# Optimization experiments

Measured on AMD Instinct MI355X. Metric: run time of the kernel, lower is better.

## Reference

```python
import jax, jax.numpy as jnp
import numpy as np

N = 100000      # nodes
E = 1600000     # edges (avg degree 16)
F_N, F_E, H = 5, 3, 64
L = 3           # num GCN layers


def setup_inputs() -> dict:
    key = jax.random.key(0)
    ks = jax.random.split(key, 20)
    s = 0.05
    p = lambda k, shape: jax.random.normal(k, shape, jnp.float32) * s
    return {
        "x": jax.random.normal(ks[0], (N, F_N), jnp.float32),
        "edge_index": jax.random.randint(ks[1], (2, E), 0, N, dtype=jnp.int32),
        "edge_attr": jax.random.normal(ks[2], (E, F_E), jnp.float32),
        # node / edge encoders
        "Wn": p(ks[3], (F_N, H)), "bn": jnp.zeros((H,), jnp.float32),
        "We": p(ks[4], (F_E, H)), "be": jnp.zeros((H,), jnp.float32),
        # stacked GCNConv weights [L, H, H] and biases [L, H]
        "Wc": p(ks[5], (L, H, H)), "bc": jnp.zeros((L, H), jnp.float32),
        # demand forecast head
        "Wd1": p(ks[6], (H, H // 2)), "bd1": jnp.zeros((H // 2,), jnp.float32),
        "Wd2": p(ks[7], (H // 2, 1)), "bd2": jnp.zeros((1,), jnp.float32),
        # inventory optimizer head
        "Wi1": p(ks[8], (H, H // 2)), "bi1": jnp.zeros((H // 2,), jnp.float32),
        "Wi2": p(ks[9], (H // 2, 1)), "bi2": jnp.zeros((1,), jnp.float32),
    }


def reference(x, edge_index, edge_attr, Wn, bn, We, be, Wc, bc,
              Wd1, bd1, Wd2, bd2, Wi1, bi1, Wi2, bi2):
    src, dst = edge_index[0], edge_index[1]
    n = x.shape[0]

    h = jax.nn.relu(x @ Wn + bn)                      # [N, H]
    _ea = jax.nn.relu(edge_attr @ We + be)            # encoded edge feats (GCNConv ignores them)

    # GCN symmetric normalization with self-loops: deg[i] = in_degree(i) + 1
    ones_e = jnp.ones(src.shape[0], h.dtype)
    deg = jax.ops.segment_sum(ones_e, dst, num_segments=n) + 1.0
    dinv = jax.lax.rsqrt(deg)                         # [N]
    norm_e = dinv[src] * dinv[dst]                    # [E]
    norm_self = (dinv * dinv)[:, None]                # [N, 1]

    for l in range(Wc.shape[0]):
        hw = h @ Wc[l]                                # [N, H]
        msgs = norm_e[:, None] * hw[src]              # gather + scale, [E, H]
        agg = jax.ops.segment_sum(msgs, dst, num_segments=n) + norm_self * hw
        h = jax.nn.relu(agg + bc[l])

    demand = jax.nn.relu(h @ Wd1 + bd1) @ Wd2 + bd2   # [N, 1]
    inventory = jax.nn.relu(h @ Wi1 + bi1) @ Wi2 + bi2
    return demand, inventory
```

## Files before the change

### kernel.cpp

```cpp
#include <hip/hip_runtime.h>

#define H 64
#define FN 5
#define EPB 4096
#define BSHIFT 8
#define CAP2 4864

typedef _Float16 half4 __attribute__((ext_vector_type(4)));
typedef _Float16 half8 __attribute__((ext_vector_type(8)));
typedef float    float8v __attribute__((ext_vector_type(8)));

__global__ void k_bscatter2(const int* __restrict__ src, const int* __restrict__ dst,
                            int* __restrict__ lofs_g, int* __restrict__ bcounts,
                            int* __restrict__ binned, int nE, int nbB) {
    __shared__ int lh[512], lpos[512], lcur[512], tmp[256];
    __shared__ int stage[EPB];
    int t = threadIdx.x;
    int e0 = blockIdx.x * EPB;
    int es[16], ed[16];
    lh[t] = 0; lh[t + 256] = 0;
    __syncthreads();
#pragma unroll
    for (int i = 0; i < 16; ++i) {
        int e = e0 + i * 256 + t;
        bool v = e < nE;
        es[i] = v ? src[e] : 0;
        ed[i] = v ? dst[e] : -1;
        if (v) atomicAdd(&lh[ed[i] >> BSHIFT], 1);
    }
    __syncthreads();
    int a0 = lh[2 * t], a1 = lh[2 * t + 1];
    tmp[t] = a0 + a1;
    __syncthreads();
    for (int s = 1; s < 256; s <<= 1) {
        int a = (t >= s) ? tmp[t - s] : 0;
        __syncthreads();
        tmp[t] += a;
        __syncthreads();
    }
    int ex = tmp[t] - (a0 + a1);
    lpos[2 * t] = ex;
    lpos[2 * t + 1] = ex + a0;
    __syncthreads();
    lcur[t] = lpos[t]; lcur[t + 256] = lpos[t + 256];
    size_t row = (size_t)blockIdx.x * (nbB + 1);
    for (int b = t; b <= nbB; b += 256) lofs_g[row + b] = lpos[b];
    for (int b = t; b < nbB; b += 256) if (lh[b]) atomicAdd(&bcounts[b], lh[b]);
    __syncthreads();
#pragma unroll
    for (int i = 0; i < 16; ++i) {
        if (ed[i] >= 0) {
            int b = ed[i] >> BSHIFT;
            int p = atomicAdd(&lcur[b], 1);
            stage[p] = es[i] | ((ed[i] & 255) << 17);
        }
    }
    __syncthreads();
    int total = lpos[nbB];
    for (int j = t; j < total; j += 256) binned[e0 + j] = stage[j];
}

__global__ void k_bscan2(const int* __restrict__ bcounts, int* __restrict__ bbase, int nbB) {
    __shared__ int tmp[512];
    int t = threadIdx.x;
    int v = (t < nbB) ? bcounts[t] : 0;
    tmp[t] = v;
    __syncthreads();
    for (int s = 1; s < 512; s <<= 1) {
        int a = (t >= s) ? tmp[t - s] : 0;
        __syncthreads();
        tmp[t] += a;
        __syncthreads();
    }
    if (t < nbB) bbase[t + 1] = tmp[t];
    if (t == 0) bbase[0] = 0;
}

__global__ void k_bcsr2(const int* __restrict__ binned, const int* __restrict__ lofs_g,
                        const int* __restrict__ bbase, int* __restrict__ row_ptr,
                        int* __restrict__ csr_src, float* __restrict__ dinv,
                        int n, int nE, int nbE, int nbB) {
    __shared__ int len_s[512], start_s[512], roff[512], tmp[256];
    __shared__ int deg[256], st[256], cur[256];
    __shared__ int lbuf[CAP2];
    __shared__ int stage2[CAP2];
    int t = threadIdx.x;
    int B = blockIdx.x;
    int node0 = B << BSHIFT;
    int nn = min(256, n - node0);
    len_s[t] = 0; len_s[t + 256] = 0;
    __syncthreads();
    for (int sb = t; sb < nbE; sb += 256) {
        size_t row = (size_t)sb * (nbB + 1);
        int o0 = lofs_g[row + B], o1 = lofs_g[row + B + 1];
        len_s[sb] = o1 - o0;
        start_s[sb] = sb * EPB + o0;
    }
    __syncthreads();
    int a0 = len_s[2 * t], a1 = len_s[2 * t + 1];
    tmp[t] = a0 + a1;
    __syncthreads();
    for (int s = 1; s < 256; s <<= 1) {
        int a = (t >= s) ? tmp[t - s] : 0;
        __syncthreads();
        tmp[t] += a;
        __syncthreads();
    }
    int ex = tmp[t] - (a0 + a1);
    roff[2 * t] = ex;
    roff[2 * t + 1] = ex + a0;
    __syncthreads();
    int total = min(roff[511] + len_s[511], CAP2);
    for (int sb = t; sb < nbE; sb += 256) {
        int s0 = start_s[sb], ln = len_s[sb], d0 = roff[sb];
        for (int k = 0; k < ln; ++k) {
            int d = d0 + k;
            if (d < CAP2) lbuf[d] = binned[s0 + k];
        }
    }
    deg[t] = 0;
    __syncthreads();
    for (int i = t; i < total; i += 256) atomicAdd(&deg[(lbuf[i] >> 17) & 255], 1);
    __syncthreads();
    tmp[t] = deg[t];
    __syncthreads();
    for (int s = 1; s < 256; s <<= 1) {
        int a = (t >= s) ? tmp[t - s] : 0;
        __syncthreads();
        tmp[t] += a;
        __syncthreads();
    }
    st[t] = tmp[t] - deg[t];
    cur[t] = st[t];
    __syncthreads();
    int base = bbase[B];
    if (t < nn) {
        row_ptr[node0 + t] = base + st[t];
        dinv[node0 + t] = 1.0f / sqrtf((float)deg[t] + 1.0f);
    }
    if (B == 0 && t == 0) row_ptr[n] = nE;
    for (int i = t; i < total; i += 256) {
        int p0 = lbuf[i];
        int p = atomicAdd(&cur[(p0 >> 17) & 255], 1);
        int sv = p0 & 0x1FFFF;
        if (p < CAP2) stage2[p] = sv;
        else csr_src[base + p] = sv;
    }
    __syncthreads();
    for (int i = t; i < total; i += 256) csr_src[base + i] = stage2[i];
}

__global__ void k_enc(const float* __restrict__ x, const float* __restrict__ Wn,
                      const float* __restrict__ bn, const float* __restrict__ dinv,
                      _Float16* __restrict__ g0, int n) {
    int tid = blockIdx.x * 256 + threadIdx.x;
    int node = tid >> 6, ch = tid & 63;
    if (node >= n) return;
    float acc = bn[ch];
#pragma unroll
    for (int k = 0; k < FN; ++k)
        acc += x[(size_t)node * FN + k] * Wn[k * H + ch];
    g0[(size_t)node * H + ch] = (_Float16)(fmaxf(acc, 0.f) * dinv[node]);
}

__global__ void k_layer(const _Float16* __restrict__ gin, const int* __restrict__ csr_src,
                        const int* __restrict__ row_ptr, const float* __restrict__ dinv,
                        const float* __restrict__ W, const float* __restrict__ bias,
                        _Float16* __restrict__ gout, float* __restrict__ hout,
                        int n, int last) {
    __shared__ float As[64 * 68];
    __shared__ int rp_s[65];
    __shared__ float dv_s[64];
    int t = threadIdx.x;
    int wave = t >> 6, lane = t & 63;
    int base = blockIdx.x * 64;
    if (t < 65) rp_s[t] = row_ptr[min(base + t, n)];
    if (t >= 128 && t < 192) {
        int nd = base + (t - 128);
        dv_s[t - 128] = (nd < n) ? dinv[nd] : 0.f;
    }
    __syncthreads();

    int c8 = (lane >> 3) * 8;
    int slot = lane & 7;
    for (int it = 0; it < 8; ++it) {
        int rA = it * 8 + wave, rB = rA + 4;
        int nodeA = base + rA, nodeB = base + rB;
        float8v accA = 0.f, accB = 0.f;
        int iA = rp_s[rA], eA = rp_s[rA + 1];
        int iB = rp_s[rB], eB = rp_s[rB + 1];
        while (iA + 8 <= eA && iB + 8 <= eB) {
            int xA = csr_src[iA + slot];
            int xB = csr_src[iB + slot];
            half8 vA = *(const half8*)(gin + (size_t)xA * H + c8);
            half8 vB = *(const half8*)(gin + (size_t)xB * H + c8);
#pragma unroll
            for (int k = 0; k < 8; ++k) { accA[k] += (float)vA[k]; accB[k] += (float)vB[k]; }
            iA += 8; iB += 8;
        }
        while (iA + 8 <= eA) {
            int xA = csr_src[iA + slot];
            half8 vA = *(const half8*)(gin + (size_t)xA * H + c8);
#pragma unroll
            for (int k = 0; k < 8; ++k) accA[k] += (float)vA[k];
            iA += 8;
        }
        while (iB + 8 <= eB) {
            int xB = csr_src[iB + slot];
            half8 vB = *(const half8*)(gin + (size_t)xB * H + c8);
#pragma unroll
            for (int k = 0; k < 8; ++k) accB[k] += (float)vB[k];
            iB += 8;
        }
        if (iA + slot < eA) {
            int xA = csr_src[iA + slot];
            half8 vA = *(const half8*)(gin + (size_t)xA * H + c8);
#pragma unroll
            for (int k = 0; k < 8; ++k) accA[k] += (float)vA[k];
        }
        if (iB + slot < eB) {
            int xB = csr_src[iB + slot];
            half8 vB = *(const half8*)(gin + (size_t)xB * H + c8);
#pragma unroll
            for (int k = 0; k < 8; ++k) accB[k] += (float)vB[k];
        }
#pragma unroll
        for (int m = 1; m <= 4; m <<= 1) {
#pragma unroll
            for (int k = 0; k < 8; ++k) {
                accA[k] += __shfl_xor(accA[k], m, 64);
                accB[k] += __shfl_xor(accB[k], m, 64);
            }
        }
        if (slot == 0) {
            float oA[8], oB[8];
            if (nodeA < n) {
                half8 sA = *(const half8*)(gin + (size_t)nodeA * H + c8);
                float dA = dv_s[rA];
#pragma unroll
                for (int k = 0; k < 8; ++k) oA[k] = (accA[k] + (float)sA[k]) * dA;
            } else {
#pragma unroll
                for (int k = 0; k < 8; ++k) oA[k] = 0.f;
            }
            if (nodeB < n) {
                half8 sB = *(const half8*)(gin + (size_t)nodeB * H + c8);
                float dB = dv_s[rB];
#pragma unroll
                for (int k = 0; k < 8; ++k) oB[k] = (accB[k] + (float)sB[k]) * dB;
            } else {
#pragma unroll
                for (int k = 0; k < 8; ++k) oB[k] = 0.f;
            }
            *(float4*)&As[rA * 68 + c8]     = make_float4(oA[0], oA[1], oA[2], oA[3]);
            *(float4*)&As[rA * 68 + c8 + 4] = make_float4(oA[4], oA[5], oA[6], oA[7]);
            *(float4*)&As[rB * 68 + c8]     = make_float4(oB[0], oB[1], oB[2], oB[3]);
            *(float4*)&As[rB * 68 + c8 + 4] = make_float4(oB[4], oB[5], oB[6], oB[7]);
        }
    }
    __syncthreads();

    int tx = t & 15, ty = t >> 4;
    int c0 = tx * 4;
    const float* a0 = As + (ty * 4 + 0) * 68;
    const float* a1 = As + (ty * 4 + 1) * 68;
    const float* a2 = As + (ty * 4 + 2) * 68;
    const float* a3 = As + (ty * 4 + 3) * 68;
    float4 acc0 = make_float4(0.f, 0.f, 0.f, 0.f);
    float4 acc1 = acc0, acc2 = acc0, acc3 = acc0;
#pragma unroll 16
    for (int k = 0; k < H; ++k) {
        float4 w = *(const float4*)(W + k * H + c0);
        float v0 = a0[k], v1 = a1[k], v2 = a2[k], v3 = a3[k];
        acc0.x += v0 * w.x; acc0.y += v0 * w.y; acc0.z += v0 * w.z; acc0.w += v0 * w.w;
        acc1.x += v1 * w.x; acc1.y += v1 * w.y; acc1.z += v1 * w.z; acc1.w += v1 * w.w;
        acc2.x += v2 * w.x; acc2.y += v2 * w.y; acc2.z += v2 * w.z; acc2.w += v2 * w.w;
        acc3.x += v3 * w.x; acc3.y += v3 * w.y; acc3.z += v3 * w.z; acc3.w += v3 * w.w;
    }
    float4 b = *(const float4*)(bias + c0);
    float4 accs[4] = {acc0, acc1, acc2, acc3};
#pragma unroll
    for (int rr = 0; rr < 4; ++rr) {
        int r = ty * 4 + rr;
        int row = base + r;
        if (row < n) {
            float4 o;
            o.x = fmaxf(accs[rr].x + b.x, 0.f);
            o.y = fmaxf(accs[rr].y + b.y, 0.f);
            o.z = fmaxf(accs[rr].z + b.z, 0.f);
            o.w = fmaxf(accs[rr].w + b.w, 0.f);
            if (last) {
                *(float4*)(hout + (size_t)row * H + c0) = o;
            } else {
                float d = dv_s[r];
                half4 hh;
                hh.x = (_Float16)(o.x * d);
                hh.y = (_Float16)(o.y * d);
                hh.z = (_Float16)(o.z * d);
                hh.w = (_Float16)(o.w * d);
                *(half4*)(gout + (size_t)row * H + c0) = hh;
            }
        }
    }
}

__global__ void k_heads(const float* __restrict__ h,
                        const float* __restrict__ Wd1, const float* __restrict__ bd1,
                        const float* __restrict__ Wd2, const float* __restrict__ bd2,
                        const float* __restrict__ Wi1, const float* __restrict__ bi1,
                        const float* __restrict__ Wi2, const float* __restrict__ bi2,
                        float* __restrict__ out, int n) {
    __shared__ float hs[64 * 65];
    int lane = threadIdx.x;
    int base = blockIdx.x * 64;
    for (int r = 0; r < 64; ++r) {
        int row = base + r;
        hs[r * 65 + lane] = (row < n) ? h[(size_t)row * H + lane] : 0.f;
    }
    __syncthreads();

    float accd[32], acci[32];
#pragma unroll
    for (int j = 0; j < 32; ++j) { accd[j] = bd1[j]; acci[j] = bi1[j]; }
    for (int k = 0; k < H; ++k) {
        float hk = hs[lane * 65 + k];
#pragma unroll
        for (int j = 0; j < 32; ++j) {
            accd[j] += hk * Wd1[k * 32 + j];
            acci[j] += hk * Wi1[k * 32 + j];
        }
    }
    float demand = bd2[0], inventory = bi2[0];
#pragma unroll
    for (int j = 0; j < 32; ++j) {
        demand    += fmaxf(accd[j], 0.f) * Wd2[j];
        inventory += fmaxf(acci[j], 0.f) * Wi2[j];
    }
    int node = base + lane;
    if (node < n) {
        out[node] = demand;
        out[n + node] = inventory;
    }
}

extern "C" void kernel_launch(void* const* d_in, const int* in_sizes, int n_in,
                              void* d_out, int out_size, void* d_ws, size_t ws_size,
                              hipStream_t stream) {
    const float* x   = (const float*)d_in[0];
    const int*   ei  = (const int*)  d_in[1];
    const float* Wn  = (const float*)d_in[3];
    const float* bn  = (const float*)d_in[4];
    const float* Wc  = (const float*)d_in[7];
    const float* bc  = (const float*)d_in[8];
    const float* Wd1 = (const float*)d_in[9];
    const float* bd1 = (const float*)d_in[10];
    const float* Wd2 = (const float*)d_in[11];
    const float* bd2 = (const float*)d_in[12];
    const float* Wi1 = (const float*)d_in[13];
    const float* bi1 = (const float*)d_in[14];
    const float* Wi2 = (const float*)d_in[15];
    const float* bi2 = (const float*)d_in[16];

    const int n  = in_sizes[0] / FN;
    const int nE = in_sizes[1] / 2;
    const int* src = ei;
    const int* dst = ei + nE;

    const int nbE = (nE + EPB - 1) / EPB;
    const int nbB = (n + 255) >> BSHIFT;
    const int nbL = (n + 63) / 64;

    char* w = (char*)d_ws;
    int* binned    = (int*)w;   w += (size_t)nbE * EPB * 4;
    int* csr_src   = (int*)w;   w += (size_t)nE * 4;
    int* row_ptr   = (int*)w;   w += (size_t)(n + 4) * 4;
    float* dinv    = (float*)w; w += (size_t)n * 4;
    int* lofs      = (int*)w;   w += (size_t)nbE * (nbB + 1) * 4;
    int* bcounts   = (int*)w;   w += 512 * 4;
    int* bbase     = (int*)w;   w += 516 * 4;
    float* hbuf    = (float*)w; w += (size_t)n * H * 4;
    _Float16* gA   = (_Float16*)w; w += (size_t)n * H * 2;
    _Float16* gB   = (_Float16*)w; w += (size_t)n * H * 2;

    hipMemsetAsync(bcounts, 0, 512 * 4, stream);

    k_bscatter2<<<nbE, 256, 0, stream>>>(src, dst, lofs, bcounts, binned, nE, nbB);
    k_bscan2   <<<1,   512, 0, stream>>>(bcounts, bbase, nbB);
    k_bcsr2    <<<nbB, 256, 0, stream>>>(binned, lofs, bbase, row_ptr, csr_src,
                                         dinv, n, nE, nbE, nbB);

    k_enc<<<((size_t)n * 64 + 255) / 256, 256, 0, stream>>>(x, Wn, bn, dinv, gA, n);

    k_layer<<<nbL, 256, 0, stream>>>(gA, csr_src, row_ptr, dinv, Wc,
                                     bc, gB, hbuf, n, 0);
    k_layer<<<nbL, 256, 0, stream>>>(gB, csr_src, row_ptr, dinv, Wc + (size_t)H * H,
                                     bc + H, gA, hbuf, n, 0);
    k_layer<<<nbL, 256, 0, stream>>>(gA, csr_src, row_ptr, dinv, Wc + (size_t)2 * H * H,
                                     bc + 2 * H, gB, hbuf, n, 1);

    k_heads<<<(n + 63) / 64, 64, 0, stream>>>(hbuf, Wd1, bd1, Wd2, bd2,
                                              Wi1, bi1, Wi2, bi2, (float*)d_out, n);
}
```

Measured before the change: 388.2 us.

## Fuse output heads into last GCN layer, widen blocks, stage edge indices in LDS

The prediction heads now run inside the final layer kernel, which removes the fp32 hidden buffer write and read and one launch. Each layer kernel runs 512 threads per 64-node block, and the block's CSR source indices are staged in shared memory when they fit within a fixed capacity, with a fallback to global reads otherwise. The dense 64x64 transform is rebalanced to two rows per thread with vectorised LDS reads. This raises shared memory and register demand per block, which may limit occupancy.

```diff
diff --git a/kernel.cpp b/kernel.cpp
--- a/kernel.cpp
+++ b/kernel.cpp
@@ -5,6 +5,7 @@
 #define EPB 4096
 #define BSHIFT 8
 #define CAP2 4864
+#define CAPE 2560
 
 typedef _Float16 half4 __attribute__((ext_vector_type(4)));
 typedef _Float16 half8 __attribute__((ext_vector_type(8)));
@@ -163,16 +164,66 @@
     g0[(size_t)node * H + ch] = (_Float16)(fmaxf(acc, 0.f) * dinv[node]);
 }
 
-__global__ void k_layer(const _Float16* __restrict__ gin, const int* __restrict__ csr_src,
-                        const int* __restrict__ row_ptr, const float* __restrict__ dinv,
-                        const float* __restrict__ W, const float* __restrict__ bias,
-                        _Float16* __restrict__ gout, float* __restrict__ hout,
-                        int n, int last) {
+__device__ __forceinline__ void gather_pair(const int* __restrict__ idx,
+                                            const _Float16* __restrict__ gin,
+                                            int iA, int eA, int iB, int eB,
+                                            int slot, int c8,
+                                            float8v& accA, float8v& accB) {
+    while (iA + 8 <= eA && iB + 8 <= eB) {
+        int xA = idx[iA + slot];
+        int xB = idx[iB + slot];
+        half8 vA = *(const half8*)(gin + (size_t)xA * H + c8);
+        half8 vB = *(const half8*)(gin + (size_t)xB * H + c8);
+#pragma unroll
+        for (int k = 0; k < 8; ++k) { accA[k] += (float)vA[k]; accB[k] += (float)vB[k]; }
+        iA += 8; iB += 8;
+    }
+    while (iA + 8 <= eA) {
+        int xA = idx[iA + slot];
+        half8 vA = *(const half8*)(gin + (size_t)xA * H + c8);
+#pragma unroll
+        for (int k = 0; k < 8; ++k) accA[k] += (float)vA[k];
+        iA += 8;
+    }
+    while (iB + 8 <= eB) {
+        int xB = idx[iB + slot];
+        half8 vB = *(const half8*)(gin + (size_t)xB * H + c8);
+#pragma unroll
+        for (int k = 0; k < 8; ++k) accB[k] += (float)vB[k];
+        iB += 8;
+    }
+    if (iA + slot < eA) {
+        int xA = idx[iA + slot];
+        half8 vA = *(const half8*)(gin + (size_t)xA * H + c8);
+#pragma unroll
+        for (int k = 0; k < 8; ++k) accA[k] += (float)vA[k];
+    }
+    if (iB + slot < eB) {
+        int xB = idx[iB + slot];
+        half8 vB = *(const half8*)(gin + (size_t)xB * H + c8);
+#pragma unroll
+        for (int k = 0; k < 8; ++k) accB[k] += (float)vB[k];
+    }
+}
+
+#define FMA4(ACC, S, WV) ACC.x += (S)*(WV).x; ACC.y += (S)*(WV).y; \
+                         ACC.z += (S)*(WV).z; ACC.w += (S)*(WV).w;
+
+__global__ __launch_bounds__(512, 8)
+void k_layer(const _Float16* __restrict__ gin, const int* __restrict__ csr_src,
+             const int* __restrict__ row_ptr, const float* __restrict__ dinv,
+             const float* __restrict__ W, const float* __restrict__ bias,
+             _Float16* __restrict__ gout, int n, int last,
+             const float* __restrict__ Wd1, const float* __restrict__ bd1,
+             const float* __restrict__ Wd2, const float* __restrict__ bd2,
+             const float* __restrict__ Wi1, const float* __restrict__ bi1,
+             const float* __restrict__ Wi2, const float* __restrict__ bi2,
+             float* __restrict__ out) {
     __shared__ float As[64 * 68];
     __shared__ int rp_s[65];
     __shared__ float dv_s[64];
+    __shared__ int eidx[CAPE];
     int t = threadIdx.x;
-    int wave = t >> 6, lane = t & 63;
     int base = blockIdx.x * 64;
     if (t < 65) rp_s[t] = row_ptr[min(base + t, n)];
     if (t >= 128 && t < 192) {
@@ -180,50 +231,25 @@
         dv_s[t - 128] = (nd < n) ? dinv[nd] : 0.f;
     }
     __syncthreads();
-
+    int e0 = rp_s[0];
+    int total = rp_s[64] - e0;
+    bool stg = (total <= CAPE);
+    if (stg)
+        for (int i = t; i < total; i += 512) eidx[i] = csr_src[e0 + i];
+    __syncthreads();
+
+    int wave = t >> 6, lane = t & 63;
     int c8 = (lane >> 3) * 8;
     int slot = lane & 7;
-    for (int it = 0; it < 8; ++it) {
-        int rA = it * 8 + wave, rB = rA + 4;
+    for (int it = 0; it < 4; ++it) {
+        int rA = it * 16 + wave, rB = rA + 8;
         int nodeA = base + rA, nodeB = base + rB;
         float8v accA = 0.f, accB = 0.f;
-        int iA = rp_s[rA], eA = rp_s[rA + 1];
-        int iB = rp_s[rB], eB = rp_s[rB + 1];
-        while (iA + 8 <= eA && iB + 8 <= eB) {
-            int xA = csr_src[iA + slot];
-            int xB = csr_src[iB + slot];
-            half8 vA = *(const half8*)(gin + (size_t)xA * H + c8);
-            half8 vB = *(const half8*)(gin + (size_t)xB * H + c8);
-#pragma unroll
-            for (int k = 0; k < 8; ++k) { accA[k] += (float)vA[k]; accB[k] += (float)vB[k]; }
-            iA += 8; iB += 8;
-        }
-        while (iA + 8 <= eA) {
-            int xA = csr_src[iA + slot];
-            half8 vA = *(const half8*)(gin + (size_t)xA * H + c8);
-#pragma unroll
-            for (int k = 0; k < 8; ++k) accA[k] += (float)vA[k];
-            iA += 8;
-        }
-        while (iB + 8 <= eB) {
-            int xB = csr_src[iB + slot];
-            half8 vB = *(const half8*)(gin + (size_t)xB * H + c8);
-#pragma unroll
-            for (int k = 0; k < 8; ++k) accB[k] += (float)vB[k];
-            iB += 8;
-        }
-        if (iA + slot < eA) {
-            int xA = csr_src[iA + slot];
-            half8 vA = *(const half8*)(gin + (size_t)xA * H + c8);
-#pragma unroll
-            for (int k = 0; k < 8; ++k) accA[k] += (float)vA[k];
-        }
-        if (iB + slot < eB) {
-            int xB = csr_src[iB + slot];
-            half8 vB = *(const half8*)(gin + (size_t)xB * H + c8);
-#pragma unroll
-            for (int k = 0; k < 8; ++k) accB[k] += (float)vB[k];
-        }
+        int iA = rp_s[rA], eAe = rp_s[rA + 1];
+        int iB = rp_s[rB], eBe = rp_s[rB + 1];
+        if (stg) gather_pair(eidx, gin, iA - e0, eAe - e0, iB - e0, eBe - e0,
+                             slot, c8, accA, accB);
+        else     gather_pair(csr_src, gin, iA, eAe, iB, eBe, slot, c8, accA, accB);
 #pragma unroll
         for (int m = 1; m <= 4; m <<= 1) {
 #pragma unroll
@@ -262,84 +288,75 @@
 
     int tx = t & 15, ty = t >> 4;
     int c0 = tx * 4;
-    const float* a0 = As + (ty * 4 + 0) * 68;
-    const float* a1 = As + (ty * 4 + 1) * 68;
-    const float* a2 = As + (ty * 4 + 2) * 68;
-    const float* a3 = As + (ty * 4 + 3) * 68;
+    int r0 = ty * 2, r1 = r0 + 1;
+    const float* a0 = As + r0 * 68;
+    const float* a1 = As + r1 * 68;
     float4 acc0 = make_float4(0.f, 0.f, 0.f, 0.f);
-    float4 acc1 = acc0, acc2 = acc0, acc3 = acc0;
-#pragma unroll 16
-    for (int k = 0; k < H; ++k) {
-        float4 w = *(const float4*)(W + k * H + c0);
-        float v0 = a0[k], v1 = a1[k], v2 = a2[k], v3 = a3[k];
-        acc0.x += v0 * w.x; acc0.y += v0 * w.y; acc0.z += v0 * w.z; acc0.w += v0 * w.w;
-        acc1.x += v1 * w.x; acc1.y += v1 * w.y; acc1.z += v1 * w.z; acc1.w += v1 * w.w;
-        acc2.x += v2 * w.x; acc2.y += v2 * w.y; acc2.z += v2 * w.z; acc2.w += v2 * w.w;
-        acc3.x += v3 * w.x; acc3.y += v3 * w.y; acc3.z += v3 * w.z; acc3.w += v3 * w.w;
+    float4 acc1 = acc0;
+#pragma unroll 4
+    for (int k = 0; k < H; k += 4) {
+        float4 av0 = *(const float4*)(a0 + k);
+        float4 av1 = *(const float4*)(a1 + k);
+        const float* wp = W + k * H + c0;
+        float4 w0 = *(const float4*)(wp);
+        float4 w1 = *(const float4*)(wp + H);
+        float4 w2 = *(const float4*)(wp + 2 * H);
+        float4 w3 = *(const float4*)(wp + 3 * H);
+        FMA4(acc0, av0.x, w0) FMA4(acc0, av0.y, w1) FMA4(acc0, av0.z, w2) FMA4(acc0, av0.w, w3)
+        FMA4(acc1, av1.x, w0) FMA4(acc1, av1.y, w1) FMA4(acc1, av1.z, w2) FMA4(acc1, av1.w, w3)
     }
     float4 b = *(const float4*)(bias + c0);
-    float4 accs[4] = {acc0, acc1, acc2, acc3};
-#pragma unroll
-    for (int rr = 0; rr < 4; ++rr) {
-        int r = ty * 4 + rr;
-        int row = base + r;
-        if (row < n) {
-            float4 o;
-            o.x = fmaxf(accs[rr].x + b.x, 0.f);
-            o.y = fmaxf(accs[rr].y + b.y, 0.f);
-            o.z = fmaxf(accs[rr].z + b.z, 0.f);
-            o.w = fmaxf(accs[rr].w + b.w, 0.f);
-            if (last) {
-                *(float4*)(hout + (size_t)row * H + c0) = o;
-            } else {
-                float d = dv_s[r];
-                half4 hh;
-                hh.x = (_Float16)(o.x * d);
-                hh.y = (_Float16)(o.y * d);
-                hh.z = (_Float16)(o.z * d);
-                hh.w = (_Float16)(o.w * d);
-                *(half4*)(gout + (size_t)row * H + c0) = hh;
-            }
-        }
-    }
-}
-
-__global__ void k_heads(const float* __restrict__ h,
-                        const float* __restrict__ Wd1, const float* __restrict__ bd1,
-                        const float* __restrict__ Wd2, const float* __restrict__ bd2,
-                        const float* __restrict__ Wi1, const float* __restrict__ bi1,
-                        const float* __restrict__ Wi2, const float* __restrict__ bi2,
-                        float* __restrict__ out, int n) {
-    __shared__ float hs[64 * 65];
-    int lane = threadIdx.x;
-    int base = blockIdx.x * 64;
-    for (int r = 0; r < 64; ++r) {
-        int row = base + r;
-        hs[r * 65 + lane] = (row < n) ? h[(size_t)row * H + lane] : 0.f;
-    }
-    __syncthreads();
-
-    float accd[32], acci[32];
-#pragma unroll
-    for (int j = 0; j < 32; ++j) { accd[j] = bd1[j]; acci[j] = bi1[j]; }
-    for (int k = 0; k < H; ++k) {
-        float hk = hs[lane * 65 + k];
-#pragma unroll
-        for (int j = 0; j < 32; ++j) {
-            accd[j] += hk * Wd1[k * 32 + j];
-            acci[j] += hk * Wi1[k * 32 + j];
-        }
-    }
-    float demand = bd2[0], inventory = bi2[0];
-#pragma unroll
-    for (int j = 0; j < 32; ++j) {
-        demand    += fmaxf(accd[j], 0.f) * Wd2[j];
-        inventory += fmaxf(acci[j], 0.f) * Wi2[j];
-    }
-    int node = base + lane;
-    if (node < n) {
-        out[node] = demand;
-        out[n + node] = inventory;
+    float4 o0, o1;
+    o0.x = fmaxf(acc0.x + b.x, 0.f); o0.y = fmaxf(acc0.y + b.y, 0.f);
+    o0.z = fmaxf(acc0.z + b.z, 0.f); o0.w = fmaxf(acc0.w + b.w, 0.f);
+    o1.x = fmaxf(acc1.x + b.x, 0.f); o1.y = fmaxf(acc1.y + b.y, 0.f);
+    o1.z = fmaxf(acc1.z + b.z, 0.f); o1.w = fmaxf(acc1.w + b.w, 0.f);
+
+    if (!last) {
+        if (base + r0 < n) {
+            float d = dv_s[r0];
+            half4 hh;
+            hh.x = (_Float16)(o0.x * d); hh.y = (_Float16)(o0.y * d);
+            hh.z = (_Float16)(o0.z * d); hh.w = (_Float16)(o0.w * d);
+            *(half4*)(gout + (size_t)(base + r0) * H + c0) = hh;
+        }
+        if (base + r1 < n) {
+            float d = dv_s[r1];
+            half4 hh;
+            hh.x = (_Float16)(o1.x * d); hh.y = (_Float16)(o1.y * d);
+            hh.z = (_Float16)(o1.z * d); hh.w = (_Float16)(o1.w * d);
+            *(half4*)(gout + (size_t)(base + r1) * H + c0) = hh;
+        }
+    } else {
+        __syncthreads();
+        *(float4*)(As + r0 * 68 + c0) = o0;
+        *(float4*)(As + r1 * 68 + c0) = o1;
+        __syncthreads();
+        int nl = t >> 3, sub = t & 7, j0 = sub * 4;
+        int node = base + nl;
+        float4 ad = *(const float4*)(bd1 + j0);
+        float4 ai = *(const float4*)(bi1 + j0);
+        const float* hrow = As + nl * 68;
+#pragma unroll 4
+        for (int k = 0; k < H; ++k) {
+            float hk = hrow[k];
+            float4 wd = *(const float4*)(Wd1 + k * 32 + j0);
+            float4 wi = *(const float4*)(Wi1 + k * 32 + j0);
+            FMA4(ad, hk, wd)
+            FMA4(ai, hk, wi)
+        }
+        float4 w2d = *(const float4*)(Wd2 + j0);
+        float4 w2i = *(const float4*)(Wi2 + j0);
+        float dp = fmaxf(ad.x, 0.f) * w2d.x + fmaxf(ad.y, 0.f) * w2d.y
+                 + fmaxf(ad.z, 0.f) * w2d.z + fmaxf(ad.w, 0.f) * w2d.w;
+        float ip = fmaxf(ai.x, 0.f) * w2i.x + fmaxf(ai.y, 0.f) * w2i.y
+                 + fmaxf(ai.z, 0.f) * w2i.z + fmaxf(ai.w, 0.f) * w2i.w;
+        dp += __shfl_xor(dp, 1, 64); dp += __shfl_xor(dp, 2, 64); dp += __shfl_xor(dp, 4, 64);
+        ip += __shfl_xor(ip, 1, 64); ip += __shfl_xor(ip, 2, 64); ip += __shfl_xor(ip, 4, 64);
+        if (sub == 0 && node < n) {
+            out[node] = dp + bd2[0];
+            out[n + node] = ip + bi2[0];
+        }
     }
 }
 
@@ -378,7 +395,6 @@
     int* lofs      = (int*)w;   w += (size_t)nbE * (nbB + 1) * 4;
     int* bcounts   = (int*)w;   w += 512 * 4;
     int* bbase     = (int*)w;   w += 516 * 4;
-    float* hbuf    = (float*)w; w += (size_t)n * H * 4;
     _Float16* gA   = (_Float16*)w; w += (size_t)n * H * 2;
     _Float16* gB   = (_Float16*)w; w += (size_t)n * H * 2;
 
@@ -391,13 +407,13 @@
 
     k_enc<<<((size_t)n * 64 + 255) / 256, 256, 0, stream>>>(x, Wn, bn, dinv, gA, n);
 
-    k_layer<<<nbL, 256, 0, stream>>>(gA, csr_src, row_ptr, dinv, Wc,
-                                     bc, gB, hbuf, n, 0);
-    k_layer<<<nbL, 256, 0, stream>>>(gB, csr_src, row_ptr, dinv, Wc + (size_t)H * H,
-                                     bc + H, gA, hbuf, n, 0);
-    k_layer<<<nbL, 256, 0, stream>>>(gA, csr_src, row_ptr, dinv, Wc + (size_t)2 * H * H,
-                                     bc + 2 * H, gB, hbuf, n, 1);
-
-    k_heads<<<(n + 63) / 64, 64, 0, stream>>>(hbuf, Wd1, bd1, Wd2, bd2,
-                                              Wi1, bi1, Wi2, bi2, (float*)d_out, n);
-}
+    float* outp = (float*)d_out;
+    k_layer<<<nbL, 512, 0, stream>>>(gA, csr_src, row_ptr, dinv, Wc, bc, gB, n, 0,
+                                     Wd1, bd1, Wd2, bd2, Wi1, bi1, Wi2, bi2, outp);
+    k_layer<<<nbL, 512, 0, stream>>>(gB, csr_src, row_ptr, dinv, Wc + (size_t)H * H,
+                                     bc + H, gA, n, 0,
+                                     Wd1, bd1, Wd2, bd2, Wi1, bi1, Wi2, bi2, outp);
+    k_layer<<<nbL, 512, 0, stream>>>(gA, csr_src, row_ptr, dinv, Wc + (size_t)2 * H * H,
+                                     bc + 2 * H, gB, n, 1,
+                                     Wd1, bd1, Wd2, bd2, Wi1, bi1, Wi2, bi2, outp);
+}
```

New measurement: 423.5 us. 1.09x slower.

## Fuse demand and inventory heads into last GCN layer epilogue

Applied to the files above, without the earlier changes.

The final GCN layer no longer writes the fp32 hidden state to a global buffer. Instead it stages the post-ReLU tile in shared memory and computes both MLP heads in place, with four threads per node and shuffle reductions. This removes a separate head kernel launch and an N×64 fp32 write and read round trip. In exchange it adds two extra barriers and a longer epilogue to the last layer kernel, which may raise register pressure.

```diff
diff --git a/kernel.cpp b/kernel.cpp
--- a/kernel.cpp
+++ b/kernel.cpp
@@ -163,11 +163,18 @@
     g0[(size_t)node * H + ch] = (_Float16)(fmaxf(acc, 0.f) * dinv[node]);
 }
 
+#define FMA4(ACC, S, WV) ACC.x += (S)*(WV).x; ACC.y += (S)*(WV).y; \
+                         ACC.z += (S)*(WV).z; ACC.w += (S)*(WV).w;
+
 __global__ void k_layer(const _Float16* __restrict__ gin, const int* __restrict__ csr_src,
                         const int* __restrict__ row_ptr, const float* __restrict__ dinv,
                         const float* __restrict__ W, const float* __restrict__ bias,
-                        _Float16* __restrict__ gout, float* __restrict__ hout,
-                        int n, int last) {
+                        _Float16* __restrict__ gout, int n, int last,
+                        const float* __restrict__ Wd1, const float* __restrict__ bd1,
+                        const float* __restrict__ Wd2, const float* __restrict__ bd2,
+                        const float* __restrict__ Wi1, const float* __restrict__ bi1,
+                        const float* __restrict__ Wi2, const float* __restrict__ bi2,
+                        float* __restrict__ out) {
     __shared__ float As[64 * 68];
     __shared__ int rp_s[65];
     __shared__ float dv_s[64];
@@ -279,67 +286,71 @@
     }
     float4 b = *(const float4*)(bias + c0);
     float4 accs[4] = {acc0, acc1, acc2, acc3};
+    float4 os[4];
 #pragma unroll
     for (int rr = 0; rr < 4; ++rr) {
-        int r = ty * 4 + rr;
-        int row = base + r;
-        if (row < n) {
-            float4 o;
-            o.x = fmaxf(accs[rr].x + b.x, 0.f);
-            o.y = fmaxf(accs[rr].y + b.y, 0.f);
-            o.z = fmaxf(accs[rr].z + b.z, 0.f);
-            o.w = fmaxf(accs[rr].w + b.w, 0.f);
-            if (last) {
-                *(float4*)(hout + (size_t)row * H + c0) = o;
-            } else {
+        os[rr].x = fmaxf(accs[rr].x + b.x, 0.f);
+        os[rr].y = fmaxf(accs[rr].y + b.y, 0.f);
+        os[rr].z = fmaxf(accs[rr].z + b.z, 0.f);
+        os[rr].w = fmaxf(accs[rr].w + b.w, 0.f);
+    }
+
+    if (!last) {
+#pragma unroll
+        for (int rr = 0; rr < 4; ++rr) {
+            int r = ty * 4 + rr;
+            int row = base + r;
+            if (row < n) {
                 float d = dv_s[r];
                 half4 hh;
-                hh.x = (_Float16)(o.x * d);
-                hh.y = (_Float16)(o.y * d);
-                hh.z = (_Float16)(o.z * d);
-                hh.w = (_Float16)(o.w * d);
+                hh.x = (_Float16)(os[rr].x * d);
+                hh.y = (_Float16)(os[rr].y * d);
+                hh.z = (_Float16)(os[rr].z * d);
+                hh.w = (_Float16)(os[rr].w * d);
                 *(half4*)(gout + (size_t)row * H + c0) = hh;
             }
         }
-    }
-}
-
-__global__ void k_heads(const float* __restrict__ h,
-                        const float* __restrict__ Wd1, const float* __restrict__ bd1,
-                        const float* __restrict__ Wd2, const float* __restrict__ bd2,
-                        const float* __restrict__ Wi1, const float* __restrict__ bi1,
-                        const float* __restrict__ Wi2, const float* __restrict__ bi2,
-                        float* __restrict__ out, int n) {
-    __shared__ float hs[64 * 65];
-    int lane = threadIdx.x;
-    int base = blockIdx.x * 64;
-    for (int r = 0; r < 64; ++r) {
-        int row = base + r;
-        hs[r * 65 + lane] = (row < n) ? h[(size_t)row * H + lane] : 0.f;
-    }
-    __syncthreads();
-
-    float accd[32], acci[32];
-#pragma unroll
-    for (int j = 0; j < 32; ++j) { accd[j] = bd1[j]; acci[j] = bi1[j]; }
-    for (int k = 0; k < H; ++k) {
-        float hk = hs[lane * 65 + k];
-#pragma unroll
-        for (int j = 0; j < 32; ++j) {
-            accd[j] += hk * Wd1[k * 32 + j];
-            acci[j] += hk * Wi1[k * 32 + j];
-        }
-    }
-    float demand = bd2[0], inventory = bi2[0];
-#pragma unroll
-    for (int j = 0; j < 32; ++j) {
-        demand    += fmaxf(accd[j], 0.f) * Wd2[j];
-        inventory += fmaxf(acci[j], 0.f) * Wi2[j];
-    }
-    int node = base + lane;
-    if (node < n) {
-        out[node] = demand;
-        out[n + node] = inventory;
+    } else {
+        __syncthreads();
+#pragma unroll
+        for (int rr = 0; rr < 4; ++rr)
+            *(float4*)(As + (ty * 4 + rr) * 68 + c0) = os[rr];
+        __syncthreads();
+        int nl = t >> 2, sub = t & 3, j0 = sub * 8;
+        int node = base + nl;
+        float4 ad0 = *(const float4*)(bd1 + j0);
+        float4 ad1 = *(const float4*)(bd1 + j0 + 4);
+        float4 ai0 = *(const float4*)(bi1 + j0);
+        float4 ai1 = *(const float4*)(bi1 + j0 + 4);
+        const float* hrow = As + nl * 68;
+#pragma unroll 4
+        for (int k = 0; k < H; ++k) {
+            float hk = hrow[k];
+            float4 wd0 = *(const float4*)(Wd1 + k * 32 + j0);
+            float4 wd1v = *(const float4*)(Wd1 + k * 32 + j0 + 4);
+            float4 wi0 = *(const float4*)(Wi1 + k * 32 + j0);
+            float4 wi1v = *(const float4*)(Wi1 + k * 32 + j0 + 4);
+            FMA4(ad0, hk, wd0) FMA4(ad1, hk, wd1v)
+            FMA4(ai0, hk, wi0) FMA4(ai1, hk, wi1v)
+        }
+        float4 w2d0 = *(const float4*)(Wd2 + j0);
+        float4 w2d1 = *(const float4*)(Wd2 + j0 + 4);
+        float4 w2i0 = *(const float4*)(Wi2 + j0);
+        float4 w2i1 = *(const float4*)(Wi2 + j0 + 4);
+        float dp = fmaxf(ad0.x, 0.f) * w2d0.x + fmaxf(ad0.y, 0.f) * w2d0.y
+                 + fmaxf(ad0.z, 0.f) * w2d0.z + fmaxf(ad0.w, 0.f) * w2d0.w
+                 + fmaxf(ad1.x, 0.f) * w2d1.x + fmaxf(ad1.y, 0.f) * w2d1.y
+                 + fmaxf(ad1.z, 0.f) * w2d1.z + fmaxf(ad1.w, 0.f) * w2d1.w;
+        float ip = fmaxf(ai0.x, 0.f) * w2i0.x + fmaxf(ai0.y, 0.f) * w2i0.y
+                 + fmaxf(ai0.z, 0.f) * w2i0.z + fmaxf(ai0.w, 0.f) * w2i0.w
+                 + fmaxf(ai1.x, 0.f) * w2i1.x + fmaxf(ai1.y, 0.f) * w2i1.y
+                 + fmaxf(ai1.z, 0.f) * w2i1.z + fmaxf(ai1.w, 0.f) * w2i1.w;
+        dp += __shfl_xor(dp, 1, 64); dp += __shfl_xor(dp, 2, 64);
+        ip += __shfl_xor(ip, 1, 64); ip += __shfl_xor(ip, 2, 64);
+        if (sub == 0 && node < n) {
+            out[node] = dp + bd2[0];
+            out[n + node] = ip + bi2[0];
+        }
     }
 }
 
@@ -378,7 +389,6 @@
     int* lofs      = (int*)w;   w += (size_t)nbE * (nbB + 1) * 4;
     int* bcounts   = (int*)w;   w += 512 * 4;
     int* bbase     = (int*)w;   w += 516 * 4;
-    float* hbuf    = (float*)w; w += (size_t)n * H * 4;
     _Float16* gA   = (_Float16*)w; w += (size_t)n * H * 2;
     _Float16* gB   = (_Float16*)w; w += (size_t)n * H * 2;
 
@@ -391,13 +401,13 @@
 
     k_enc<<<((size_t)n * 64 + 255) / 256, 256, 0, stream>>>(x, Wn, bn, dinv, gA, n);
 
-    k_layer<<<nbL, 256, 0, stream>>>(gA, csr_src, row_ptr, dinv, Wc,
-                                     bc, gB, hbuf, n, 0);
+    float* outp = (float*)d_out;
+    k_layer<<<nbL, 256, 0, stream>>>(gA, csr_src, row_ptr, dinv, Wc, bc, gB, n, 0,
+                                     Wd1, bd1, Wd2, bd2, Wi1, bi1, Wi2, bi2, outp);
     k_layer<<<nbL, 256, 0, stream>>>(gB, csr_src, row_ptr, dinv, Wc + (size_t)H * H,
-                                     bc + H, gA, hbuf, n, 0);
+                                     bc + H, gA, n, 0,
+                                     Wd1, bd1, Wd2, bd2, Wi1, bi1, Wi2, bi2, outp);
     k_layer<<<nbL, 256, 0, stream>>>(gA, csr_src, row_ptr, dinv, Wc + (size_t)2 * H * H,
-                                     bc + 2 * H, gB, hbuf, n, 1);
-
-    k_heads<<<(n + 63) / 64, 64, 0, stream>>>(hbuf, Wd1, bd1, Wd2, bd2,
-                                              Wi1, bi1, Wi2, bi2, (float*)d_out, n);
-}
+                                     bc + 2 * H, gB, n, 1,
+                                     Wd1, bd1, Wd2, bd2, Wi1, bi1, Wi2, bi2, outp);
+}
```

Measured after the change: 466.1 us. +20.1%, slower.
